# Performance work log

Hardware: AMD Instinct MI355X
Metric: run time of the kernel (lower is better)

The kernel has to match this reference:

```python
import jax, jax.numpy as jnp
import numpy as np

NUM_HEADS = 4
SPLIT_SIZE = 8  # idx == 1 -> H_sp = H, W_sp = split_size (vertical stripe windows)


def setup_inputs() -> dict:
    key = jax.random.key(0)
    k1, k2, k3 = jax.random.split(key, 3)
    temp = jax.random.normal(k1, (16, 3, 128, 64, 64), dtype=jnp.float32)
    conv_w = jax.random.normal(k2, (128, 1, 3, 3), dtype=jnp.float32) * 0.1  # depthwise LePE conv
    conv_b = jax.random.normal(k3, (128,), dtype=jnp.float32) * 0.1
    return {"temp": temp, "conv_w": conv_w, "conv_b": conv_b}


def reference(temp, conv_w, conv_b):
    B, _, C, H, W = temp.shape
    H_sp, W_sp = H, SPLIT_SIZE          # idx == 1 cross-shaped window
    # H % H_sp == 0 and W % W_sp == 0 -> F.pad amounts are zero here
    nH, nW = H // H_sp, W // W_sp
    L = H_sp * W_sp                     # tokens per window
    hd = C // NUM_HEADS
    scale = hd ** -0.5

    q, k, v = temp[:, 0], temp[:, 1], temp[:, 2]  # each [B, C, H, W]

    def im2cswin(x):
        # img2windows: B C H W -> (B*nH*nW, L, C) then split heads -> (Bw, nh, L, hd)
        x = x.reshape(B, C, nH, H_sp, nW, W_sp).transpose(0, 2, 4, 3, 5, 1)
        x = x.reshape(-1, L, NUM_HEADS, hd).transpose(0, 2, 1, 3)
        return x

    qw = im2cswin(q) * scale            # (Bw, nh, L, hd)
    kw = im2cswin(k)

    # get_rpe: window-partition v as images, depthwise 3x3 conv for LePE
    vimg = v.reshape(B, C, nH, H_sp, nW, W_sp).transpose(0, 2, 4, 1, 3, 5)
    vimg = vimg.reshape(-1, C, H_sp, W_sp)  # (Bw, C, H_sp, W_sp)
    rpe = jax.lax.conv_general_dilated(
        vimg, conv_w, window_strides=(1, 1), padding="SAME",
        dimension_numbers=("NCHW", "OIHW", "NCHW"), feature_group_count=C,
    ) + conv_b[None, :, None, None]
    rpe = rpe.reshape(-1, NUM_HEADS, hd, L).transpose(0, 1, 3, 2)  # (Bw, nh, L, hd)
    vw = vimg.reshape(-1, NUM_HEADS, hd, L).transpose(0, 1, 3, 2)

    attn = jax.nn.softmax(jnp.einsum("wnld,wnmd->wnlm", qw, kw), axis=-1)
    out = jnp.einsum("wnlm,wnmd->wnld", attn, vw) + rpe  # (Bw, nh, L, hd)

    out = out.transpose(0, 2, 1, 3).reshape(-1, L, C)    # (Bw, L, C)
    # windows2img: (Bw, L, C) -> (B, H, W, C)
    out = out.reshape(B, nH, nW, H_sp, W_sp, C).transpose(0, 1, 3, 2, 4, 5)
    out = out.reshape(B, H, W, C)
    return out.reshape(B, H * W, C)
```

## Files before the change

### kernel.cpp

```cpp
#include <hip/hip_runtime.h>

typedef __attribute__((ext_vector_type(8))) short short8;
typedef __attribute__((ext_vector_type(2))) float float2_t;
typedef __attribute__((ext_vector_type(4))) float float4_t;
typedef __attribute__((ext_vector_type(4))) int int4_t;
typedef __attribute__((ext_vector_type(2))) unsigned uint2_t;
typedef __attribute__((ext_vector_type(4))) unsigned uint4_t;

#define CH_STRIDE 4096
#define IMG_STRIDE 524288
#define HW 4096
#define V520 520

static __device__ __forceinline__ float bitsf(unsigned u) { return __builtin_bit_cast(float, u); }
static __device__ __forceinline__ unsigned bitsu(float f) { return __builtin_bit_cast(unsigned, f); }

static __device__ __forceinline__ unsigned cvt_pk(float lo, float hi) {
    unsigned r;
    asm("v_cvt_pk_bf16_f32 %0, %1, %2" : "=v"(r) : "v"(lo), "v"(hi));
    return r;
}

__global__ __launch_bounds__(1024) void cswin_fused(
    const float* __restrict__ temp, const float* __restrict__ cw,
    const float* __restrict__ cb, float* __restrict__ out)
{
    __shared__ short Kc[64 * 40];
    __shared__ short Vt[32 * V520];

    int bx = blockIdx.x;
    int nw = bx >> 6;
    int r  = bx & 63;
    int b  = r >> 2;
    int n  = r & 3;

    int t    = threadIdx.x;
    int wv   = t >> 6;
    int lane = t & 63;
    int mr   = lane & 15;
    int q    = lane >> 4;

    const float* tq = temp + (size_t)b * 3 * IMG_STRIDE + (size_t)(n * 32) * CH_STRIDE + nw * 8;
    const float* tk = tq + IMG_STRIDE;
    const float* tv = tk + IMG_STRIDE;

    int row0 = wv * 32;
    const float qscale = 0.2550348889072310f;

    short8 Qf[2];
    #pragma unroll
    for (int qt = 0; qt < 2; ++qt) {
        int l = row0 + qt * 16 + mr;
        int sp = (l >> 3) * 64 + (l & 7);
        float f[8];
        #pragma unroll
        for (int j = 0; j < 8; ++j)
            f[j] = tq[(q * 8 + j) * CH_STRIDE + sp] * qscale;
        uint4_t up = { cvt_pk(f[0], f[1]), cvt_pk(f[2], f[3]),
                       cvt_pk(f[4], f[5]), cvt_pk(f[6], f[7]) };
        Qf[qt] = __builtin_bit_cast(short8, up);
    }

    float4_t zero4 = {0.f, 0.f, 0.f, 0.f};
    float4_t acc[2][2];
    #pragma unroll
    for (int dt = 0; dt < 2; ++dt)
        #pragma unroll
        for (int qt = 0; qt < 2; ++qt)
            acc[dt][qt] = zero4;
    float lsum[2] = {0.f, 0.f};

    int ld  = t >> 5;
    int seg = t & 31;
    const float* tkld = tk + (size_t)ld * CH_STRIDE;
    const float* tvld = tv + (size_t)ld * CH_STRIDE;

    float kx[2], vx[2];
    #pragma unroll
    for (int i = 0; i < 2; ++i) {
        int lb = seg + 32 * i;
        int sp = (lb >> 3) * 64 + (lb & 7);
        kx[i] = tkld[sp]; vx[i] = tvld[sp];
    }
    {
        unsigned pk = cvt_pk(kx[0], kx[1]);
        Kc[(seg)      * 40 + ld] = (short)(pk & 0xffffu);
        Kc[(seg + 32) * 40 + ld] = (short)(pk >> 16);
        unsigned pv = cvt_pk(vx[0], vx[1]);
        Vt[ld * V520 + seg]      = (short)(pv & 0xffffu);
        Vt[ld * V520 + seg + 32] = (short)(pv >> 16);
    }
    #pragma unroll
    for (int i = 0; i < 2; ++i) {
        int lb = 64 + seg + 32 * i;
        int sp = (lb >> 3) * 64 + (lb & 7);
        kx[i] = tkld[sp]; vx[i] = tvld[sp];
    }

    #pragma unroll 1
    for (int ch = 0; ch < 8; ++ch) {
        __syncthreads();

        #pragma unroll
        for (int g = 0; g < 2; ++g) {
            short8 KaA = *reinterpret_cast<const short8*>(&Kc[((2 * g) * 16 + mr) * 40 + q * 8]);
            short8 KaB = *reinterpret_cast<const short8*>(&Kc[((2 * g + 1) * 16 + mr) * 40 + q * 8]);
            unsigned pa0[2], pa1[2], pb0[2], pb1[2];
            #pragma unroll
            for (int qt = 0; qt < 2; ++qt) {
                float4_t sA = __builtin_amdgcn_mfma_f32_16x16x32_bf16(KaA, Qf[qt], zero4, 0, 0, 0);
                float4_t sB = __builtin_amdgcn_mfma_f32_16x16x32_bf16(KaB, Qf[qt], zero4, 0, 0, 0);
                float eA0 = __builtin_amdgcn_exp2f(sA.x), eA1 = __builtin_amdgcn_exp2f(sA.y);
                float eA2 = __builtin_amdgcn_exp2f(sA.z), eA3 = __builtin_amdgcn_exp2f(sA.w);
                float eB0 = __builtin_amdgcn_exp2f(sB.x), eB1 = __builtin_amdgcn_exp2f(sB.y);
                float eB2 = __builtin_amdgcn_exp2f(sB.z), eB3 = __builtin_amdgcn_exp2f(sB.w);
                lsum[qt] += ((eA0 + eA1) + (eA2 + eA3)) + ((eB0 + eB1) + (eB2 + eB3));
                pa0[qt] = __builtin_amdgcn_perm(bitsu(eA1), bitsu(eA0), 0x07060302u);
                pa1[qt] = __builtin_amdgcn_perm(bitsu(eA3), bitsu(eA2), 0x07060302u);
                pb0[qt] = __builtin_amdgcn_perm(bitsu(eB1), bitsu(eB0), 0x07060302u);
                pb1[qt] = __builtin_amdgcn_perm(bitsu(eB3), bitsu(eB2), 0x07060302u);
            }
            int base = ch * 64 + g * 32 + q * 8;
            short8 Va0 = *reinterpret_cast<const short8*>(&Vt[mr * V520 + base]);
            short8 Va1 = *reinterpret_cast<const short8*>(&Vt[(16 + mr) * V520 + base]);
            #pragma unroll
            for (int qt = 0; qt < 2; ++qt) {
                uint2_t re = __builtin_amdgcn_permlane32_swap(pa0[qt], pb0[qt], 0, 0);
                uint2_t we = __builtin_amdgcn_permlane16_swap(re.x, re.y, 0, 0);
                uint2_t ro = __builtin_amdgcn_permlane32_swap(pa1[qt], pb1[qt], 0, 0);
                uint2_t wo = __builtin_amdgcn_permlane16_swap(ro.x, ro.y, 0, 0);
                int4_t pi = { (int)we.x, (int)wo.x, (int)we.y, (int)wo.y };
                short8 Pb = __builtin_bit_cast(short8, pi);
                acc[0][qt] = __builtin_amdgcn_mfma_f32_16x16x32_bf16(Va0, Pb, acc[0][qt], 0, 0, 0);
                acc[1][qt] = __builtin_amdgcn_mfma_f32_16x16x32_bf16(Va1, Pb, acc[1][qt], 0, 0, 0);
            }
        }

        if (ch < 7) {
            __syncthreads();
            {
                unsigned pk = cvt_pk(kx[0], kx[1]);
                Kc[(seg)      * 40 + ld] = (short)(pk & 0xffffu);
                Kc[(seg + 32) * 40 + ld] = (short)(pk >> 16);
                unsigned pv = cvt_pk(vx[0], vx[1]);
                Vt[ld * V520 + (ch + 1) * 64 + seg]      = (short)(pv & 0xffffu);
                Vt[ld * V520 + (ch + 1) * 64 + seg + 32] = (short)(pv >> 16);
            }
            if (ch < 6) {
                #pragma unroll
                for (int i = 0; i < 2; ++i) {
                    int lb = (ch + 2) * 64 + seg + 32 * i;
                    int sp = (lb >> 3) * 64 + (lb & 7);
                    kx[i] = tkld[sp]; vx[i] = tvld[sp];
                }
            }
        }
    }

    float inv[2];
    #pragma unroll
    for (int qt = 0; qt < 2; ++qt) {
        float v = lsum[qt];
        v += __shfl_xor(v, 16);
        v += __shfl_xor(v, 32);
        inv[qt] = 1.0f / v;
    }

    float* outb = out + (size_t)b * HW * 128 + nw * 8 * 128 + n * 32;
    #pragma unroll
    for (int qt = 0; qt < 2; ++qt) {
        int l = row0 + qt * 16 + mr;
        size_t basep = (size_t)((l >> 3) * 64 + (l & 7)) * 128;
        #pragma unroll
        for (int dt = 0; dt < 2; ++dt) {
            float4_t o = acc[dt][qt] * inv[qt];
            *reinterpret_cast<float4_t*>(outb + basep + dt * 16 + q * 4) = o;
        }
    }

    __syncthreads();

    int c2 = (t & 15) * 2;
    int h  = t >> 4;
    float2_t outv[8];
    #pragma unroll
    for (int cc = 0; cc < 2; ++cc) {
        int c = c2 + cc;
        float w9[9];
        #pragma unroll
        for (int i = 0; i < 9; ++i) w9[i] = cw[(n * 32 + c) * 9 + i];
        float bias = cb[n * 32 + c];
        float rv[3][8];
        #pragma unroll
        for (int rr = 0; rr < 3; ++rr) {
            int hh = h - 1 + rr;
            if (hh >= 0 && hh < 64) {
                short8 u = *reinterpret_cast<const short8*>(&Vt[c * V520 + hh * 8]);
                #pragma unroll
                for (int j = 0; j < 8; ++j)
                    rv[rr][j] = bitsf(((unsigned)(unsigned short)u[j]) << 16);
            } else {
                #pragma unroll
                for (int j = 0; j < 8; ++j) rv[rr][j] = 0.f;
            }
        }
        #pragma unroll
        for (int w = 0; w < 8; ++w) {
            float o = bias;
            #pragma unroll
            for (int rr = 0; rr < 3; ++rr) {
                if (w > 0) o += rv[rr][w - 1] * w9[rr * 3 + 0];
                o += rv[rr][w] * w9[rr * 3 + 1];
                if (w < 7) o += rv[rr][w + 1] * w9[rr * 3 + 2];
            }
            outv[w][cc] = o;
        }
    }
    #pragma unroll
    for (int w = 0; w < 8; ++w) {
        size_t off = (size_t)h * 8192 + w * 128 + c2;
        float2_t cur = *reinterpret_cast<const float2_t*>(outb + off);
        cur += outv[w];
        *reinterpret_cast<float2_t*>(outb + off) = cur;
    }
}

extern "C" void kernel_launch(void* const* d_in, const int* in_sizes, int n_in,
                              void* d_out, int out_size, void* d_ws, size_t ws_size,
                              hipStream_t stream) {
    const float* temp = (const float*)d_in[0];
    const float* cw   = (const float*)d_in[1];
    const float* cb   = (const float*)d_in[2];
    float* out = (float*)d_out;
    hipLaunchKernelGGL(cswin_fused, dim3(512), dim3(1024), 0, stream, temp, cw, cb, out);
}
```

Baseline: 186.5 us.

## Process K/V chunks in pairs with double-buffered K tile and staggered wave order

Doubles the K staging buffer so two 64-key chunks are resident per phase, halving the number of block-wide barriers (4 phases instead of 8). Odd and even waves process the two chunks in opposite order, so concurrent waves read different LDS buffers and bank contention is spread out. Global loads now prefetch two chunks ahead, which raises register use and LDS footprint slightly.

```diff
diff --git a/kernel.cpp b/kernel.cpp
--- a/kernel.cpp
+++ b/kernel.cpp
@@ -25,7 +25,7 @@
     const float* __restrict__ temp, const float* __restrict__ cw,
     const float* __restrict__ cb, float* __restrict__ out)
 {
-    __shared__ short Kc[64 * 40];
+    __shared__ short Kc[2][64 * 40];
     __shared__ short Vt[32 * V520];
 
     int bx = blockIdx.x;
@@ -75,83 +75,112 @@
     const float* tkld = tk + (size_t)ld * CH_STRIDE;
     const float* tvld = tv + (size_t)ld * CH_STRIDE;
 
-    float kx[2], vx[2];
+    float kx0[2], vx0[2], kx1[2], vx1[2];
     #pragma unroll
     for (int i = 0; i < 2; ++i) {
-        int lb = seg + 32 * i;
-        int sp = (lb >> 3) * 64 + (lb & 7);
-        kx[i] = tkld[sp]; vx[i] = tvld[sp];
+        int lb0 = seg + 32 * i;
+        int sp0 = (lb0 >> 3) * 64 + (lb0 & 7);
+        kx0[i] = tkld[sp0]; vx0[i] = tvld[sp0];
+        int lb1 = 64 + seg + 32 * i;
+        int sp1 = (lb1 >> 3) * 64 + (lb1 & 7);
+        kx1[i] = tkld[sp1]; vx1[i] = tvld[sp1];
     }
     {
-        unsigned pk = cvt_pk(kx[0], kx[1]);
-        Kc[(seg)      * 40 + ld] = (short)(pk & 0xffffu);
-        Kc[(seg + 32) * 40 + ld] = (short)(pk >> 16);
-        unsigned pv = cvt_pk(vx[0], vx[1]);
+        unsigned pk = cvt_pk(kx0[0], kx0[1]);
+        Kc[0][(seg)      * 40 + ld] = (short)(pk & 0xffffu);
+        Kc[0][(seg + 32) * 40 + ld] = (short)(pk >> 16);
+        unsigned pv = cvt_pk(vx0[0], vx0[1]);
         Vt[ld * V520 + seg]      = (short)(pv & 0xffffu);
         Vt[ld * V520 + seg + 32] = (short)(pv >> 16);
+        pk = cvt_pk(kx1[0], kx1[1]);
+        Kc[1][(seg)      * 40 + ld] = (short)(pk & 0xffffu);
+        Kc[1][(seg + 32) * 40 + ld] = (short)(pk >> 16);
+        pv = cvt_pk(vx1[0], vx1[1]);
+        Vt[ld * V520 + 64 + seg]      = (short)(pv & 0xffffu);
+        Vt[ld * V520 + 64 + seg + 32] = (short)(pv >> 16);
     }
     #pragma unroll
     for (int i = 0; i < 2; ++i) {
-        int lb = 64 + seg + 32 * i;
-        int sp = (lb >> 3) * 64 + (lb & 7);
-        kx[i] = tkld[sp]; vx[i] = tvld[sp];
-    }
+        int lb0 = 128 + seg + 32 * i;
+        int sp0 = (lb0 >> 3) * 64 + (lb0 & 7);
+        kx0[i] = tkld[sp0]; vx0[i] = tvld[sp0];
+        int lb1 = 192 + seg + 32 * i;
+        int sp1 = (lb1 >> 3) * 64 + (lb1 & 7);
+        kx1[i] = tkld[sp1]; vx1[i] = tvld[sp1];
+    }
+
+    int cfirst = wv & 1;
 
     #pragma unroll 1
-    for (int ch = 0; ch < 8; ++ch) {
+    for (int ph = 0; ph < 4; ++ph) {
         __syncthreads();
 
         #pragma unroll
-        for (int g = 0; g < 2; ++g) {
-            short8 KaA = *reinterpret_cast<const short8*>(&Kc[((2 * g) * 16 + mr) * 40 + q * 8]);
-            short8 KaB = *reinterpret_cast<const short8*>(&Kc[((2 * g + 1) * 16 + mr) * 40 + q * 8]);
-            unsigned pa0[2], pa1[2], pb0[2], pb1[2];
+        for (int s = 0; s < 2; ++s) {
+            int cc = 2 * ph + (cfirst ^ s);
+            const short* Kb = Kc[cc & 1];
             #pragma unroll
-            for (int qt = 0; qt < 2; ++qt) {
-                float4_t sA = __builtin_amdgcn_mfma_f32_16x16x32_bf16(KaA, Qf[qt], zero4, 0, 0, 0);
-                float4_t sB = __builtin_amdgcn_mfma_f32_16x16x32_bf16(KaB, Qf[qt], zero4, 0, 0, 0);
-                float eA0 = __builtin_amdgcn_exp2f(sA.x), eA1 = __builtin_amdgcn_exp2f(sA.y);
-                float eA2 = __builtin_amdgcn_exp2f(sA.z), eA3 = __builtin_amdgcn_exp2f(sA.w);
-                float eB0 = __builtin_amdgcn_exp2f(sB.x), eB1 = __builtin_amdgcn_exp2f(sB.y);
-                float eB2 = __builtin_amdgcn_exp2f(sB.z), eB3 = __builtin_amdgcn_exp2f(sB.w);
-                lsum[qt] += ((eA0 + eA1) + (eA2 + eA3)) + ((eB0 + eB1) + (eB2 + eB3));
-                pa0[qt] = __builtin_amdgcn_perm(bitsu(eA1), bitsu(eA0), 0x07060302u);
-                pa1[qt] = __builtin_amdgcn_perm(bitsu(eA3), bitsu(eA2), 0x07060302u);
-                pb0[qt] = __builtin_amdgcn_perm(bitsu(eB1), bitsu(eB0), 0x07060302u);
-                pb1[qt] = __builtin_amdgcn_perm(bitsu(eB3), bitsu(eB2), 0x07060302u);
-            }
-            int base = ch * 64 + g * 32 + q * 8;
-            short8 Va0 = *reinterpret_cast<const short8*>(&Vt[mr * V520 + base]);
-            short8 Va1 = *reinterpret_cast<const short8*>(&Vt[(16 + mr) * V520 + base]);
-            #pragma unroll
-            for (int qt = 0; qt < 2; ++qt) {
-                uint2_t re = __builtin_amdgcn_permlane32_swap(pa0[qt], pb0[qt], 0, 0);
-                uint2_t we = __builtin_amdgcn_permlane16_swap(re.x, re.y, 0, 0);
-                uint2_t ro = __builtin_amdgcn_permlane32_swap(pa1[qt], pb1[qt], 0, 0);
-                uint2_t wo = __builtin_amdgcn_permlane16_swap(ro.x, ro.y, 0, 0);
-                int4_t pi = { (int)we.x, (int)wo.x, (int)we.y, (int)wo.y };
-                short8 Pb = __builtin_bit_cast(short8, pi);
-                acc[0][qt] = __builtin_amdgcn_mfma_f32_16x16x32_bf16(Va0, Pb, acc[0][qt], 0, 0, 0);
-                acc[1][qt] = __builtin_amdgcn_mfma_f32_16x16x32_bf16(Va1, Pb, acc[1][qt], 0, 0, 0);
-            }
-        }
-
-        if (ch < 7) {
+            for (int g = 0; g < 2; ++g) {
+                short8 KaA = *reinterpret_cast<const short8*>(&Kb[((2 * g) * 16 + mr) * 40 + q * 8]);
+                short8 KaB = *reinterpret_cast<const short8*>(&Kb[((2 * g + 1) * 16 + mr) * 40 + q * 8]);
+                unsigned pa0[2], pa1[2], pb0[2], pb1[2];
+                #pragma unroll
+                for (int qt = 0; qt < 2; ++qt) {
+                    float4_t sA = __builtin_amdgcn_mfma_f32_16x16x32_bf16(KaA, Qf[qt], zero4, 0, 0, 0);
+                    float4_t sB = __builtin_amdgcn_mfma_f32_16x16x32_bf16(KaB, Qf[qt], zero4, 0, 0, 0);
+                    float eA0 = __builtin_amdgcn_exp2f(sA.x), eA1 = __builtin_amdgcn_exp2f(sA.y);
+                    float eA2 = __builtin_amdgcn_exp2f(sA.z), eA3 = __builtin_amdgcn_exp2f(sA.w);
+                    float eB0 = __builtin_amdgcn_exp2f(sB.x), eB1 = __builtin_amdgcn_exp2f(sB.y);
+                    float eB2 = __builtin_amdgcn_exp2f(sB.z), eB3 = __builtin_amdgcn_exp2f(sB.w);
+                    lsum[qt] += ((eA0 + eA1) + (eA2 + eA3)) + ((eB0 + eB1) + (eB2 + eB3));
+                    pa0[qt] = __builtin_amdgcn_perm(bitsu(eA1), bitsu(eA0), 0x07060302u);
+                    pa1[qt] = __builtin_amdgcn_perm(bitsu(eA3), bitsu(eA2), 0x07060302u);
+                    pb0[qt] = __builtin_amdgcn_perm(bitsu(eB1), bitsu(eB0), 0x07060302u);
+                    pb1[qt] = __builtin_amdgcn_perm(bitsu(eB3), bitsu(eB2), 0x07060302u);
+                }
+                int base = cc * 64 + g * 32 + q * 8;
+                short8 Va0 = *reinterpret_cast<const short8*>(&Vt[mr * V520 + base]);
+                short8 Va1 = *reinterpret_cast<const short8*>(&Vt[(16 + mr) * V520 + base]);
+                #pragma unroll
+                for (int qt = 0; qt < 2; ++qt) {
+                    uint2_t re = __builtin_amdgcn_permlane32_swap(pa0[qt], pb0[qt], 0, 0);
+                    uint2_t we = __builtin_amdgcn_permlane16_swap(re.x, re.y, 0, 0);
+                    uint2_t ro = __builtin_amdgcn_permlane32_swap(pa1[qt], pb1[qt], 0, 0);
+                    uint2_t wo = __builtin_amdgcn_permlane16_swap(ro.x, ro.y, 0, 0);
+                    int4_t pi = { (int)we.x, (int)wo.x, (int)we.y, (int)wo.y };
+                    short8 Pb = __builtin_bit_cast(short8, pi);
+                    acc[0][qt] = __builtin_amdgcn_mfma_f32_16x16x32_bf16(Va0, Pb, acc[0][qt], 0, 0, 0);
+                    acc[1][qt] = __builtin_amdgcn_mfma_f32_16x16x32_bf16(Va1, Pb, acc[1][qt], 0, 0, 0);
+                }
+            }
+        }
+
+        if (ph < 3) {
             __syncthreads();
             {
-                unsigned pk = cvt_pk(kx[0], kx[1]);
-                Kc[(seg)      * 40 + ld] = (short)(pk & 0xffffu);
-                Kc[(seg + 32) * 40 + ld] = (short)(pk >> 16);
-                unsigned pv = cvt_pk(vx[0], vx[1]);
-                Vt[ld * V520 + (ch + 1) * 64 + seg]      = (short)(pv & 0xffffu);
-                Vt[ld * V520 + (ch + 1) * 64 + seg + 32] = (short)(pv >> 16);
-            }
-            if (ch < 6) {
+                int ce = (2 * ph + 2) * 64, co = (2 * ph + 3) * 64;
+                unsigned pk = cvt_pk(kx0[0], kx0[1]);
+                Kc[0][(seg)      * 40 + ld] = (short)(pk & 0xffffu);
+                Kc[0][(seg + 32) * 40 + ld] = (short)(pk >> 16);
+                unsigned pv = cvt_pk(vx0[0], vx0[1]);
+                Vt[ld * V520 + ce + seg]      = (short)(pv & 0xffffu);
+                Vt[ld * V520 + ce + seg + 32] = (short)(pv >> 16);
+                pk = cvt_pk(kx1[0], kx1[1]);
+                Kc[1][(seg)      * 40 + ld] = (short)(pk & 0xffffu);
+                Kc[1][(seg + 32) * 40 + ld] = (short)(pk >> 16);
+                pv = cvt_pk(vx1[0], vx1[1]);
+                Vt[ld * V520 + co + seg]      = (short)(pv & 0xffffu);
+                Vt[ld * V520 + co + seg + 32] = (short)(pv >> 16);
+            }
+            if (ph < 2) {
                 #pragma unroll
                 for (int i = 0; i < 2; ++i) {
-                    int lb = (ch + 2) * 64 + seg + 32 * i;
-                    int sp = (lb >> 3) * 64 + (lb & 7);
-                    kx[i] = tkld[sp]; vx[i] = tvld[sp];
+                    int lb0 = (2 * ph + 4) * 64 + seg + 32 * i;
+                    int sp0 = (lb0 >> 3) * 64 + (lb0 & 7);
+                    kx0[i] = tkld[sp0]; vx0[i] = tvld[sp0];
+                    int lb1 = (2 * ph + 5) * 64 + seg + 32 * i;
+                    int sp1 = (lb1 >> 3) * 64 + (lb1 & 7);
+                    kx1[i] = tkld[sp1]; vx1[i] = tvld[sp1];
                 }
             }
         }
```

Result: slower. 204.7 us (+9.7%).
